# Optimization experiments

Hardware: AMD Instinct MI355X
Metric: run time of the kernel (lower is better)

Reference implementation:

```python
import jax, jax.numpy as jnp
import numpy as np

B, DK, N, DV = 16, 64, 8192, 64


def setup_inputs() -> dict:
    key = jax.random.key(0)
    kq, kk, kv = jax.random.split(key, 3)
    q = jax.random.normal(kq, (B, DK, N), dtype=jnp.float32)   # channel-first q
    k = jax.random.normal(kk, (B, N, DK), dtype=jnp.float32)
    v = jax.random.normal(kv, (B, N, DV), dtype=jnp.float32)
    return {"q": q, "k": k, "v": v}


def reference(q, k, v):
    # torch: bmm(q.permute(0,2,1), bmm(k.permute(0,2,1), v))
    # k^T v: [B, DK, DV] -- small on-chip-able intermediate
    ktv = jnp.einsum('bnk,bnv->bkv', k, v)
    # q^T (k^T v): [B, N, DV]
    out = jnp.einsum('bkn,bkv->bnv', q, ktv)
    return out
```

## Files before the change

kernel.cpp:

```cpp
#include <hip/hip_runtime.h>


#define B_   16
#define N_   8192
#define DK_  64
#define DV_  64
#define CH_  64

__global__ __launch_bounds__(256) void p1_partial(
    const float* __restrict__ K, const float* __restrict__ V,
    float* __restrict__ part)
{
    __shared__ float sm[4][2048];

    const int c = blockIdx.x, b = blockIdx.y, t = threadIdx.x;
    const int w = t >> 6, lane = t & 63;
    const int kk = (lane >> 3) * 8;
    const int vv = (lane & 7) * 8;
    float* Ksw = &sm[w][0];
    float* Vsw = &sm[w][1024];

    const size_t row0 = (size_t)b * N_ + (size_t)c * 128 + (size_t)w * 32;
    const float4* K4 = (const float4*)(K + row0 * DK_);
    const float4* V4 = (const float4*)(V + row0 * DV_);

    float acc[8][8] = {};

    #pragma unroll
    for (int r = 0; r < 2; ++r) {
        float4 kb_[4], vb_[4];
        #pragma unroll
        for (int j = 0; j < 4; ++j) kb_[j] = K4[r * 256 + j * 64 + lane];
        #pragma unroll
        for (int j = 0; j < 4; ++j) vb_[j] = V4[r * 256 + j * 64 + lane];
        #pragma unroll
        for (int j = 0; j < 4; ++j) {
            ((float4*)Ksw)[j * 64 + lane] = kb_[j];
            ((float4*)Vsw)[j * 64 + lane] = vb_[j];
        }
        #pragma unroll 4
        for (int n = 0; n < 16; ++n) {
            alignas(16) float fk[8], fv[8];
            *(float4*)&fk[0] = *(const float4*)&Ksw[n * 64 + kk];
            *(float4*)&fk[4] = *(const float4*)&Ksw[n * 64 + kk + 4];
            *(float4*)&fv[0] = *(const float4*)&Vsw[n * 64 + vv];
            *(float4*)&fv[4] = *(const float4*)&Vsw[n * 64 + vv + 4];
            #pragma unroll
            for (int i = 0; i < 8; ++i)
                #pragma unroll
                for (int j = 0; j < 8; ++j)
                    acc[i][j] += fk[i] * fv[j];
        }
    }

    __syncthreads();
    float* red = &sm[0][0];
    if (w == 0) {
        #pragma unroll
        for (int i = 0; i < 8; ++i) {
            *(float4*)&red[(kk + i) * 64 + vv]     = make_float4(acc[i][0], acc[i][1], acc[i][2], acc[i][3]);
            *(float4*)&red[(kk + i) * 64 + vv + 4] = make_float4(acc[i][4], acc[i][5], acc[i][6], acc[i][7]);
        }
    }
    __syncthreads();
    #pragma unroll
    for (int ww = 1; ww < 4; ++ww) {
        if (w == ww) {
            #pragma unroll
            for (int i = 0; i < 8; ++i) {
                float4 r0 = *(float4*)&red[(kk + i) * 64 + vv];
                float4 r1 = *(float4*)&red[(kk + i) * 64 + vv + 4];
                r0.x += acc[i][0]; r0.y += acc[i][1]; r0.z += acc[i][2]; r0.w += acc[i][3];
                r1.x += acc[i][4]; r1.y += acc[i][5]; r1.z += acc[i][6]; r1.w += acc[i][7];
                *(float4*)&red[(kk + i) * 64 + vv]     = r0;
                *(float4*)&red[(kk + i) * 64 + vv + 4] = r1;
            }
        }
        __syncthreads();
    }

    float4* P = (float4*)(part + ((size_t)c * B_ + b) * 4096);
    #pragma unroll
    for (int j = 0; j < 4; ++j)
        P[t + 256 * j] = ((const float4*)red)[t + 256 * j];
}

__global__ __launch_bounds__(256) void p1_reduce(
    const float* __restrict__ part, float* __restrict__ ktv)
{
    const int idx = blockIdx.x * 256 + threadIdx.x;
    float s = 0.f;
    #pragma unroll 16
    for (int c = 0; c < CH_; ++c)
        s += part[(size_t)c * 65536 + idx];
    ktv[idx] = s;
}

__global__ __launch_bounds__(256) void p2(
    const float* __restrict__ q, const float* __restrict__ ktv,
    float* __restrict__ out)
{
    __shared__ float ks[4096];

    const int nb = blockIdx.x, b = blockIdx.y, t = threadIdx.x;
    const int w = t >> 6, lane = t & 63;
    const int nl = (lane >> 3) * 4;
    const int vl = (lane & 7) * 8;
    const int n0 = nb * 128 + w * 32;

    const float4* kt4 = (const float4*)(ktv + (size_t)b * 4096);
    #pragma unroll
    for (int j = 0; j < 4; ++j)
        ((float4*)ks)[t + 256 * j] = kt4[t + 256 * j];
    __syncthreads();

    const float* ql = q + (size_t)b * DK_ * N_ + n0 + nl;

    float acc[4][8] = {};
    #pragma unroll
    for (int kb = 0; kb < 4; ++kb) {
        alignas(16) float fq[16][4];
        #pragma unroll
        for (int u = 0; u < 16; ++u)
            *(float4*)&fq[u][0] = *(const float4*)(ql + (size_t)(kb * 16 + u) * N_);
        #pragma unroll
        for (int u = 0; u < 16; ++u) {
            const int k = kb * 16 + u;
            alignas(16) float fv[8];
            *(float4*)&fv[0] = *(const float4*)&ks[k * 64 + vl];
            *(float4*)&fv[4] = *(const float4*)&ks[k * 64 + vl + 4];
            #pragma unroll
            for (int i = 0; i < 4; ++i)
                #pragma unroll
                for (int j = 0; j < 8; ++j)
                    acc[i][j] += fq[u][i] * fv[j];
        }
    }

    float* ob = out + ((size_t)b * N_ + n0 + nl) * DV_ + vl;
    #pragma unroll
    for (int i = 0; i < 4; ++i) {
        *(float4*)&ob[(size_t)i * DV_]     = make_float4(acc[i][0], acc[i][1], acc[i][2], acc[i][3]);
        *(float4*)&ob[(size_t)i * DV_ + 4] = make_float4(acc[i][4], acc[i][5], acc[i][6], acc[i][7]);
    }
}

extern "C" void kernel_launch(void* const* d_in, const int* in_sizes, int n_in,
                              void* d_out, int out_size, void* d_ws, size_t ws_size,
                              hipStream_t stream)
{
    (void)in_sizes; (void)n_in; (void)out_size; (void)ws_size;
    const float* q = (const float*)d_in[0];
    const float* k = (const float*)d_in[1];
    const float* v = (const float*)d_in[2];
    float* out = (float*)d_out;

    float* part = (float*)d_ws;
    float* ktv  = part + (size_t)CH_ * B_ * 4096;

    p1_partial<<<dim3(CH_, B_), 256, 0, stream>>>(k, v, part);
    p1_reduce<<<dim3(256), 256, 0, stream>>>(part, ktv);
    p2<<<dim3(64, B_), 256, 0, stream>>>(q, ktv, out);
}
```

Before: 151.4 us.

## Fuse three phases into one cooperative kernel with grid-wide syncs

Merges the partial K^T V, the cross-chunk reduction and the Q^T·ktv product into a single cooperative kernel of 1024 blocks separated by grid.sync, falling back to the three-kernel path if the cooperative launch fails. This removes two kernel launch gaps and their tail drains. In exchange it adds two grid-wide barriers, and it requires all 1024 blocks to be co-resident (launch_bounds 256,4). The reduction now splits its 64 chunks across 4 threads per output and combines them with shuffles.

```diff
diff --git a/kernel.cpp b/kernel.cpp
--- a/kernel.cpp
+++ b/kernel.cpp
@@ -1,4 +1,7 @@
 #include <hip/hip_runtime.h>
+#include <hip/hip_cooperative_groups.h>
+
+namespace cg = cooperative_groups;
 
 
 #define B_   16
@@ -6,6 +9,148 @@
 #define DK_  64
 #define DV_  64
 #define CH_  64
+
+__global__ __launch_bounds__(256, 4) void fused(
+    const float* __restrict__ q, const float* __restrict__ K,
+    const float* __restrict__ V, float* __restrict__ part,
+    float* __restrict__ ktv, float* __restrict__ out)
+{
+    __shared__ float sm[4][2048];
+
+    const int c = blockIdx.x, b = blockIdx.y, t = threadIdx.x;
+    const int w = t >> 6, lane = t & 63;
+
+    {
+        const int kk = (lane >> 3) * 8;
+        const int vv = (lane & 7) * 8;
+        float* Ksw = &sm[w][0];
+        float* Vsw = &sm[w][1024];
+
+        const size_t row0 = (size_t)b * N_ + (size_t)c * 128 + (size_t)w * 32;
+        const float4* K4 = (const float4*)(K + row0 * DK_);
+        const float4* V4 = (const float4*)(V + row0 * DV_);
+
+        float acc[8][8] = {};
+
+        #pragma unroll
+        for (int r = 0; r < 2; ++r) {
+            float4 kb_[4], vb_[4];
+            #pragma unroll
+            for (int j = 0; j < 4; ++j) kb_[j] = K4[r * 256 + j * 64 + lane];
+            #pragma unroll
+            for (int j = 0; j < 4; ++j) vb_[j] = V4[r * 256 + j * 64 + lane];
+            #pragma unroll
+            for (int j = 0; j < 4; ++j) {
+                ((float4*)Ksw)[j * 64 + lane] = kb_[j];
+                ((float4*)Vsw)[j * 64 + lane] = vb_[j];
+            }
+            #pragma unroll 4
+            for (int n = 0; n < 16; ++n) {
+                alignas(16) float fk[8], fv[8];
+                *(float4*)&fk[0] = *(const float4*)&Ksw[n * 64 + kk];
+                *(float4*)&fk[4] = *(const float4*)&Ksw[n * 64 + kk + 4];
+                *(float4*)&fv[0] = *(const float4*)&Vsw[n * 64 + vv];
+                *(float4*)&fv[4] = *(const float4*)&Vsw[n * 64 + vv + 4];
+                #pragma unroll
+                for (int i = 0; i < 8; ++i)
+                    #pragma unroll
+                    for (int j = 0; j < 8; ++j)
+                        acc[i][j] += fk[i] * fv[j];
+            }
+        }
+
+        __syncthreads();
+        float* red = &sm[0][0];
+        if (w == 0) {
+            #pragma unroll
+            for (int i = 0; i < 8; ++i) {
+                *(float4*)&red[(kk + i) * 64 + vv]     = make_float4(acc[i][0], acc[i][1], acc[i][2], acc[i][3]);
+                *(float4*)&red[(kk + i) * 64 + vv + 4] = make_float4(acc[i][4], acc[i][5], acc[i][6], acc[i][7]);
+            }
+        }
+        __syncthreads();
+        #pragma unroll
+        for (int ww = 1; ww < 4; ++ww) {
+            if (w == ww) {
+                #pragma unroll
+                for (int i = 0; i < 8; ++i) {
+                    float4 r0 = *(float4*)&red[(kk + i) * 64 + vv];
+                    float4 r1 = *(float4*)&red[(kk + i) * 64 + vv + 4];
+                    r0.x += acc[i][0]; r0.y += acc[i][1]; r0.z += acc[i][2]; r0.w += acc[i][3];
+                    r1.x += acc[i][4]; r1.y += acc[i][5]; r1.z += acc[i][6]; r1.w += acc[i][7];
+                    *(float4*)&red[(kk + i) * 64 + vv]     = r0;
+                    *(float4*)&red[(kk + i) * 64 + vv + 4] = r1;
+                }
+            }
+            __syncthreads();
+        }
+
+        float4* P = (float4*)(part + ((size_t)c * B_ + b) * 4096);
+        #pragma unroll
+        for (int j = 0; j < 4; ++j)
+            P[t + 256 * j] = ((const float4*)red)[t + 256 * j];
+    }
+
+    cg::this_grid().sync();
+
+    {
+        const int fb = b * 64 + c;
+        const int o  = fb * 64 + (t >> 2);
+        const int g  = t & 3;
+        float s = 0.f;
+        #pragma unroll
+        for (int u = 0; u < 16; ++u)
+            s += part[(size_t)(g * 16 + u) * 65536 + o];
+        s += __shfl_xor(s, 1);
+        s += __shfl_xor(s, 2);
+        if (g == 0) ktv[o] = s;
+    }
+
+    cg::this_grid().sync();
+
+    {
+        float* ks = &sm[0][0];
+        const int nl = (lane >> 3) * 4;
+        const int vl = (lane & 7) * 8;
+        const int n0 = c * 128 + w * 32;
+
+        const float4* kt4 = (const float4*)(ktv + (size_t)b * 4096);
+        #pragma unroll
+        for (int j = 0; j < 4; ++j)
+            ((float4*)ks)[t + 256 * j] = kt4[t + 256 * j];
+        __syncthreads();
+
+        const float* ql = q + (size_t)b * DK_ * N_ + n0 + nl;
+
+        float acc2[4][8] = {};
+        #pragma unroll
+        for (int kb = 0; kb < 4; ++kb) {
+            alignas(16) float fq[16][4];
+            #pragma unroll
+            for (int u = 0; u < 16; ++u)
+                *(float4*)&fq[u][0] = *(const float4*)(ql + (size_t)(kb * 16 + u) * N_);
+            #pragma unroll
+            for (int u = 0; u < 16; ++u) {
+                const int k = kb * 16 + u;
+                alignas(16) float fv[8];
+                *(float4*)&fv[0] = *(const float4*)&ks[k * 64 + vl];
+                *(float4*)&fv[4] = *(const float4*)&ks[k * 64 + vl + 4];
+                #pragma unroll
+                for (int i = 0; i < 4; ++i)
+                    #pragma unroll
+                    for (int j = 0; j < 8; ++j)
+                        acc2[i][j] += fq[u][i] * fv[j];
+            }
+        }
+
+        float* ob = out + ((size_t)b * N_ + n0 + nl) * DV_ + vl;
+        #pragma unroll
+        for (int i = 0; i < 4; ++i) {
+            *(float4*)&ob[(size_t)i * DV_]     = make_float4(acc2[i][0], acc2[i][1], acc2[i][2], acc2[i][3]);
+            *(float4*)&ob[(size_t)i * DV_ + 4] = make_float4(acc2[i][4], acc2[i][5], acc2[i][6], acc2[i][7]);
+        }
+    }
+}
 
 __global__ __launch_bounds__(256) void p1_partial(
     const float* __restrict__ K, const float* __restrict__ V,
@@ -158,7 +303,15 @@
     float* part = (float*)d_ws;
     float* ktv  = part + (size_t)CH_ * B_ * 4096;
 
-    p1_partial<<<dim3(CH_, B_), 256, 0, stream>>>(k, v, part);
-    p1_reduce<<<dim3(256), 256, 0, stream>>>(part, ktv);
-    p2<<<dim3(64, B_), 256, 0, stream>>>(q, ktv, out);
-}
+    void* args[] = { (void*)&q, (void*)&k, (void*)&v,
+                     (void*)&part, (void*)&ktv, (void*)&out };
+    hipError_t e = hipLaunchCooperativeKernel(
+        reinterpret_cast<void*>(fused), dim3(CH_, B_), dim3(256),
+        args, 0, stream);
+    if (e != hipSuccess) {
+        (void)hipGetLastError();
+        p1_partial<<<dim3(CH_, B_), 256, 0, stream>>>(k, v, part);
+        p1_reduce<<<dim3(256), 256, 0, stream>>>(part, ktv);
+        p2<<<dim3(64, B_), 256, 0, stream>>>(q, ktv, out);
+    }
+}
```

Result: slower. 428.5 us (+183.0%).
